# Optimization experiments

Measured on AMD Instinct MI355X. Metric: run time of the kernel, lower is better.

Reference implementation:

```python
import jax, jax.numpy as jnp
import numpy as np

N, M, NNZ, D, H = 4096, 1024, 65536, 512, 8
DH = D // H
DFF = 4 * D
EPS = 1e-5


def layer_norm(x, g, b):
    mu = jnp.mean(x, axis=-1, keepdims=True)
    var = jnp.mean((x - mu) ** 2, axis=-1, keepdims=True)
    return (x - mu) / jnp.sqrt(var + EPS) * g + b


def setup_inputs() -> dict:
    key = jax.random.key(0)
    ks = jax.random.split(key, 16)
    s = 1.0 / np.sqrt(D)
    inp = {}
    inp['x'] = jax.random.normal(ks[0], (N, D), jnp.float32)
    node = jax.random.randint(ks[1], (NNZ,), 0, N, jnp.int32)
    edge = jax.random.randint(ks[2], (NNZ,), 0, M, jnp.int32)
    inp['hyperedge_index'] = jnp.stack([node, edge], axis=0)
    inp['hyperedge_attr'] = jax.random.normal(ks[3], (M, D), jnp.float32)
    # HypergraphConv params (heads=1): lin (no bias), att [2*D], output bias
    inp['Wh'] = jax.random.normal(ks[4], (D, D), jnp.float32) * s
    inp['att'] = jax.random.normal(ks[5], (2 * D,), jnp.float32) * s
    inp['bias_h'] = jnp.zeros((D,), jnp.float32)
    # outer LayerNorms
    inp['ln1_g'] = jnp.ones((D,), jnp.float32); inp['ln1_b'] = jnp.zeros((D,), jnp.float32)
    inp['ln2_g'] = jnp.ones((D,), jnp.float32); inp['ln2_b'] = jnp.zeros((D,), jnp.float32)
    # TransformerEncoderLayer params (post-norm, relu, dropout off at eval)
    inp['in_proj_w'] = jax.random.normal(ks[6], (3 * D, D), jnp.float32) * s
    inp['in_proj_b'] = jnp.zeros((3 * D,), jnp.float32)
    inp['out_proj_w'] = jax.random.normal(ks[7], (D, D), jnp.float32) * s
    inp['out_proj_b'] = jnp.zeros((D,), jnp.float32)
    inp['ff1_w'] = jax.random.normal(ks[8], (DFF, D), jnp.float32) * s
    inp['ff1_b'] = jnp.zeros((DFF,), jnp.float32)
    inp['ff2_w'] = jax.random.normal(ks[9], (D, DFF), jnp.float32) * (1.0 / np.sqrt(DFF))
    inp['ff2_b'] = jnp.zeros((D,), jnp.float32)
    inp['tln1_g'] = jnp.ones((D,), jnp.float32); inp['tln1_b'] = jnp.zeros((D,), jnp.float32)
    inp['tln2_g'] = jnp.ones((D,), jnp.float32); inp['tln2_b'] = jnp.zeros((D,), jnp.float32)
    return inp


def hypergraph_conv(x, node, edge, hyperedge_attr, Wh, att, bias_h):
    # PyG HypergraphConv, use_attention=True, heads=1, concat=True
    xl = x @ Wh.T                      # [N, D]
    el = hyperedge_attr @ Wh.T         # [M, D]
    # per-incidence attention score
    a = xl[node] @ att[:D] + el[edge] @ att[D:]          # [NNZ]
    a = jnp.where(a >= 0, a, 0.2 * a)                    # leaky_relu(0.2)
    # scatter-softmax grouped by node index
    amax = jax.ops.segment_max(a, node, num_segments=N)
    a = jnp.exp(a - amax[node])
    den = jax.ops.segment_sum(a, node, num_segments=N)
    alpha = a / (den[node] + 1e-16)
    # degree normalizations (hyperedge_weight = ones)
    ones = jnp.ones((NNZ,), x.dtype)
    Dn = jax.ops.segment_sum(ones, node, num_segments=N)
    Dinv = jnp.where(Dn > 0, 1.0 / Dn, 0.0)
    Bn = jax.ops.segment_sum(ones, edge, num_segments=M)
    Binv = jnp.where(Bn > 0, 1.0 / Bn, 0.0)
    # node -> hyperedge aggregation
    msg1 = (Binv[edge] * alpha)[:, None] * xl[node]      # [NNZ, D]
    ef = jax.ops.segment_sum(msg1, edge, num_segments=M)  # [M, D]
    # hyperedge -> node aggregation
    msg2 = (Dinv[node] * alpha)[:, None] * ef[edge]
    out = jax.ops.segment_sum(msg2, node, num_segments=N)  # [N, D]
    return out + bias_h


def reference(x, hyperedge_index, hyperedge_attr, Wh, att, bias_h,
              ln1_g, ln1_b, ln2_g, ln2_b,
              in_proj_w, in_proj_b, out_proj_w, out_proj_b,
              ff1_w, ff1_b, ff2_w, ff2_b,
              tln1_g, tln1_b, tln2_g, tln2_b):
    node, edge = hyperedge_index[0], hyperedge_index[1]
    x_conv = hypergraph_conv(x, node, edge, hyperedge_attr, Wh, att, bias_h)
    x1 = layer_norm(x + x_conv, ln1_g, ln1_b)
    # TransformerEncoderLayer (post-norm, eval: dropout off), seq of N tokens
    qkv = x1 @ in_proj_w.T + in_proj_b
    q, k, v = jnp.split(qkv, 3, axis=-1)
    q = q.reshape(N, H, DH); k = k.reshape(N, H, DH); v = v.reshape(N, H, DH)
    scores = jnp.einsum('nhd,mhd->hnm', q, k) / np.sqrt(DH)
    attw = jax.nn.softmax(scores, axis=-1)
    ctx = jnp.einsum('hnm,mhd->nhd', attw, v).reshape(N, D)
    attn_out = ctx @ out_proj_w.T + out_proj_b
    x2 = layer_norm(x1 + attn_out, tln1_g, tln1_b)
    ff = jax.nn.relu(x2 @ ff1_w.T + ff1_b) @ ff2_w.T + ff2_b
    x3 = layer_norm(x2 + ff, tln2_g, tln2_b)
    return layer_norm(x1 + x3, ln2_g, ln2_b)
```

## Files before the change

kernel.cpp:

```cpp
#include <hip/hip_runtime.h>
#include <math.h>

#define NN   4096
#define MM   1024
#define NNZC 65536
#define DD   512
#define HH   8
#define DHH  64
#define DFFC 2048
#define NSPLIT 4

typedef short bf16x8 __attribute__((ext_vector_type(8)));
typedef float f32x4  __attribute__((ext_vector_type(4)));

static __device__ inline unsigned short f2bf(float f) {
  union { float f; unsigned int u; } v; v.f = f;
  unsigned int r = v.u + 0x7fff + ((v.u >> 16) & 1);
  return (unsigned short)(r >> 16);
}
static __device__ inline float bf2f(unsigned short u) {
  return __uint_as_float((unsigned int)u << 16);
}

__device__ inline void gload16(const void* g, void* l) {
  __builtin_amdgcn_global_load_lds(
      (const __attribute__((address_space(1))) void*)g,
      (__attribute__((address_space(3))) void*)l, 16, 0, 0);
}

__device__ inline void atomicMaxF(float* addr, float val) {
  if (val >= 0.f) atomicMax((int*)addr, __float_as_int(val));
  else            atomicMin((unsigned int*)addr, __float_as_uint(val));
}

__global__ void init_kernel(float* amax, float* den, int* DnCnt, int* BnCnt,
                            int* node_cur, int* edge_cur) {
  int i = blockIdx.x * 256 + threadIdx.x;
  if (i < NN) { amax[i] = -INFINITY; den[i] = 0.f; DnCnt[i] = 0; node_cur[i] = 0; }
  if (i < MM) { BnCnt[i] = 0; edge_cur[i] = 0; }
}

__global__ __launch_bounds__(256) void f2b_multi(
    const float* s0, unsigned short* d0, int n0,
    const float* s1, unsigned short* d1, int n1,
    const float* s2, unsigned short* d2, int n2,
    const float* s3, unsigned short* d3, int n3,
    const float* s4, unsigned short* d4, int n4,
    const float* s5, unsigned short* d5, int n5,
    const float* s6, unsigned short* d6, int n6) {
  const float* in; unsigned short* out; int n8;
  switch (blockIdx.y) {
    case 0: in=s0; out=d0; n8=n0; break;
    case 1: in=s1; out=d1; n8=n1; break;
    case 2: in=s2; out=d2; n8=n2; break;
    case 3: in=s3; out=d3; n8=n3; break;
    case 4: in=s4; out=d4; n8=n4; break;
    case 5: in=s5; out=d5; n8=n5; break;
    default: in=s6; out=d6; n8=n6; break;
  }
  for (int i = blockIdx.x*256 + threadIdx.x; i < n8; i += gridDim.x*256) {
    float4 v0 = *(const float4*)&in[(size_t)i*8];
    float4 v1 = *(const float4*)&in[(size_t)i*8 + 4];
    unsigned short w[8];
    w[0]=f2bf(v0.x); w[1]=f2bf(v0.y); w[2]=f2bf(v0.z); w[3]=f2bf(v0.w);
    w[4]=f2bf(v1.x); w[5]=f2bf(v1.y); w[6]=f2bf(v1.z); w[7]=f2bf(v1.w);
    *(ulonglong2*)&out[(size_t)i*8] = *(ulonglong2*)w;
  }
}

__global__ __launch_bounds__(256) void gemm_bt_bf16(
    const unsigned short* __restrict__ A, const unsigned short* __restrict__ B,
    const float* __restrict__ bias, float* __restrict__ Cf,
    unsigned short* __restrict__ Cb, int N, int K, int relu) {
  __shared__ __align__(16) unsigned short Al[128*64];
  __shared__ __align__(16) unsigned short Bl[128*64];
  const int t = threadIdx.x;
  const int w = t >> 6, l = t & 63;
  const int lg = l >> 4, lid = l & 15;
  const int wr = w >> 1, wc = w & 1;
  const int bm = blockIdx.x * 128, bn = blockIdx.y * 128;

  f32x4 acc[4][4];
  #pragma unroll
  for (int mi = 0; mi < 4; ++mi)
    #pragma unroll
    for (int ni = 0; ni < 4; ++ni) acc[mi][ni] = (f32x4)0.f;

  for (int k0 = 0; k0 < K; k0 += 64) {
    #pragma unroll
    for (int i = 0; i < 4; ++i) {
      int cid = i*256 + t;
      int row = cid >> 3, cp = cid & 7;
      int gc = cp ^ (row & 7);
      gload16(&A[(size_t)(bm + row)*K + k0 + gc*8], &Al[cid*8]);
      gload16(&B[(size_t)(bn + row)*K + k0 + gc*8], &Bl[cid*8]);
    }
    asm volatile("s_waitcnt vmcnt(0)" ::: "memory");
    __syncthreads();
    #pragma unroll
    for (int ks = 0; ks < 2; ++ks) {
      bf16x8 af[4], bfr[4];
      #pragma unroll
      for (int mi = 0; mi < 4; ++mi) {
        int r = wr*64 + mi*16 + lid;
        af[mi] = *(const bf16x8*)&Al[r*64 + ((ks*4 + lg) ^ (r & 7))*8];
      }
      #pragma unroll
      for (int ni = 0; ni < 4; ++ni) {
        int r = wc*64 + ni*16 + lid;
        bfr[ni] = *(const bf16x8*)&Bl[r*64 + ((ks*4 + lg) ^ (r & 7))*8];
      }
      __builtin_amdgcn_s_setprio(1);
      #pragma unroll
      for (int mi = 0; mi < 4; ++mi)
        #pragma unroll
        for (int ni = 0; ni < 4; ++ni)
          acc[mi][ni] = __builtin_amdgcn_mfma_f32_16x16x32_bf16(af[mi], bfr[ni], acc[mi][ni], 0, 0, 0);
      __builtin_amdgcn_s_setprio(0);
    }
    __syncthreads();
  }

  #pragma unroll
  for (int ni = 0; ni < 4; ++ni) {
    int col = bn + wc*64 + ni*16 + lid;
    float bv = bias ? bias[col] : 0.f;
    #pragma unroll
    for (int mi = 0; mi < 4; ++mi) {
      #pragma unroll
      for (int rg = 0; rg < 4; ++rg) {
        int row = bm + wr*64 + mi*16 + lg*4 + rg;
        float v = acc[mi][ni][rg] + bv;
        if (relu) v = fmaxf(v, 0.f);
        if (Cf) Cf[(size_t)row*N + col] = v;
        if (Cb) Cb[(size_t)row*N + col] = f2bf(v);
      }
    }
  }
}

__global__ __launch_bounds__(256) void gemm_bt_bf16_n64(
    const unsigned short* __restrict__ A, const unsigned short* __restrict__ B,
    const float* __restrict__ bias, unsigned short* __restrict__ Cb, int N, int K,
    unsigned short* __restrict__ VtbOpt) {
  __shared__ __align__(16) unsigned short Al[128*64];
  __shared__ __align__(16) unsigned short Bl[64*64];
  const int t = threadIdx.x;
  const int w = t >> 6, l = t & 63;
  const int lg = l >> 4, lid = l & 15;
  const int wr = w >> 1, wc = w & 1;
  const int bm = blockIdx.x * 128, bn = blockIdx.y * 64;

  f32x4 acc[4][2];
  #pragma unroll
  for (int mi = 0; mi < 4; ++mi)
    #pragma unroll
    for (int ni = 0; ni < 2; ++ni) acc[mi][ni] = (f32x4)0.f;

  for (int k0 = 0; k0 < K; k0 += 64) {
    #pragma unroll
    for (int i = 0; i < 4; ++i) {
      int cid = i*256 + t;
      int row = cid >> 3, cp = cid & 7;
      int gc = cp ^ (row & 7);
      gload16(&A[(size_t)(bm + row)*K + k0 + gc*8], &Al[cid*8]);
    }
    #pragma unroll
    for (int i = 0; i < 2; ++i) {
      int cid = i*256 + t;
      int row = cid >> 3, cp = cid & 7;
      int gc = cp ^ (row & 7);
      gload16(&B[(size_t)(bn + row)*K + k0 + gc*8], &Bl[cid*8]);
    }
    asm volatile("s_waitcnt vmcnt(0)" ::: "memory");
    __syncthreads();
    #pragma unroll
    for (int ks = 0; ks < 2; ++ks) {
      bf16x8 af[4], bfr[2];
      #pragma unroll
      for (int mi = 0; mi < 4; ++mi) {
        int r = wr*64 + mi*16 + lid;
        af[mi] = *(const bf16x8*)&Al[r*64 + ((ks*4 + lg) ^ (r & 7))*8];
      }
      #pragma unroll
      for (int ni = 0; ni < 2; ++ni) {
        int r = wc*32 + ni*16 + lid;
        bfr[ni] = *(const bf16x8*)&Bl[r*64 + ((ks*4 + lg) ^ (r & 7))*8];
      }
      __builtin_amdgcn_s_setprio(1);
      #pragma unroll
      for (int mi = 0; mi < 4; ++mi)
        #pragma unroll
        for (int ni = 0; ni < 2; ++ni)
          acc[mi][ni] = __builtin_amdgcn_mfma_f32_16x16x32_bf16(af[mi], bfr[ni], acc[mi][ni], 0, 0, 0);
      __builtin_amdgcn_s_setprio(0);
    }
    __syncthreads();
  }

  if (VtbOpt && bn >= 1024) {
    #pragma unroll
    for (int ni = 0; ni < 2; ++ni) {
      int col = bn + wc*32 + ni*16 + lid;
      float bv = bias ? bias[col] : 0.f;
      int d = col - 1024;
      int h = d >> 6, dd = d & 63;
      #pragma unroll
      for (int mi = 0; mi < 4; ++mi) {
        int tok0 = bm + wr*64 + mi*16 + lg*4;
        ushort4 w4;
        w4.x = f2bf(acc[mi][ni][0] + bv);
        w4.y = f2bf(acc[mi][ni][1] + bv);
        w4.z = f2bf(acc[mi][ni][2] + bv);
        w4.w = f2bf(acc[mi][ni][3] + bv);
        *(ushort4*)&VtbOpt[(size_t)h*64*NN + (size_t)dd*NN + tok0] = w4;
      }
    }
  } else {
    #pragma unroll
    for (int ni = 0; ni < 2; ++ni) {
      int col = bn + wc*32 + ni*16 + lid;
      float bv = bias ? bias[col] : 0.f;
      #pragma unroll
      for (int mi = 0; mi < 4; ++mi) {
        #pragma unroll
        for (int rg = 0; rg < 4; ++rg) {
          int row = bm + wr*64 + mi*16 + lg*4 + rg;
          Cb[(size_t)row*N + col] = f2bf(acc[mi][ni][rg] + bv);
        }
      }
    }
  }
}

__global__ __launch_bounds__(256) void rowdot_both(const unsigned short* __restrict__ xlb,
    const unsigned short* __restrict__ elb, const float* __restrict__ att,
    float* __restrict__ s_node, float* __restrict__ s_edge) {
  int w = (blockIdx.x * 256 + threadIdx.x) >> 6;
  int lane = threadIdx.x & 63;
  const unsigned short* xr;
  const float* vec;
  if (w < NN) { xr = &xlb[(size_t)w * DD]; vec = att; }
  else        { xr = &elb[(size_t)(w - NN) * DD]; vec = att + DD; }
  float s = 0.f;
  #pragma unroll
  for (int j = 0; j < 8; ++j) s += bf2f(xr[lane + 64*j]) * vec[lane + 64*j];
  #pragma unroll
  for (int off = 1; off < 64; off <<= 1) s += __shfl_xor(s, off, 64);
  if (lane == 0) {
    if (w < NN) s_node[w] = s;
    else        s_edge[w - NN] = s;
  }
}

__global__ void incidence_pass1(const int* __restrict__ node_idx, const int* __restrict__ edge_idx,
    const float* __restrict__ s_node, const float* __restrict__ s_edge,
    float* __restrict__ a_buf, float* amax, int* DnCnt, int* BnCnt) {
  int i = blockIdx.x * 256 + threadIdx.x;
  if (i >= NNZC) return;
  int n = node_idx[i], m = edge_idx[i];
  float a = s_node[n] + s_edge[m];
  a = (a >= 0.f) ? a : 0.2f * a;
  a_buf[i] = a;
  atomicMaxF(&amax[n], a);
  atomicAdd(&DnCnt[n], 1);
  atomicAdd(&BnCnt[m], 1);
}

__global__ __launch_bounds__(1024) void exscan2_kernel(const int* __restrict__ inA,
    int* __restrict__ outA, int nA, const int* __restrict__ inB, int* __restrict__ outB, int nB) {
  const int* in; int* out; int n;
  if (blockIdx.x == 0) { in = inA; out = outA; n = nA; }
  else                 { in = inB; out = outB; n = nB; }
  __shared__ int sums[1024];
  const int t = threadIdx.x;
  const int chunk = (n + 1023) >> 10;
  const int start = t * chunk;
  const int stop  = min(start + chunk, n);
  int local = 0;
  for (int i = start; i < stop; ++i) local += in[i];
  sums[t] = local;
  __syncthreads();
  for (int o = 1; o < 1024; o <<= 1) {
    int v = (t >= o) ? sums[t - o] : 0;
    __syncthreads();
    sums[t] += v;
    __syncthreads();
  }
  int run = (t == 0) ? 0 : sums[t - 1];
  for (int i = start; i < stop; ++i) { out[i] = run; run += in[i]; }
  if (t == 1023) out[n] = sums[1023];
}

__global__ void incidence_pass2(const int* __restrict__ node_idx, const int* __restrict__ edge_idx,
    float* __restrict__ a_buf, const float* __restrict__ amax, float* den,
    const int* __restrict__ node_off, const int* __restrict__ edge_off,
    int* node_cur, int* edge_cur, int* node_list, int* edge_list) {
  int i = blockIdx.x * 256 + threadIdx.x;
  if (i >= NNZC) return;
  int n = node_idx[i], m = edge_idx[i];
  float e = __expf(a_buf[i] - amax[n]);
  a_buf[i] = e;
  atomicAdd(&den[n], e);
  int pn = atomicAdd(&node_cur[n], 1);
  node_list[node_off[n] + pn] = i;
  int pm = atomicAdd(&edge_cur[m], 1);
  edge_list[edge_off[m] + pm] = i;
}

__global__ __launch_bounds__(256) void gather_edge(const int* __restrict__ edge_off,
    const int* __restrict__ edge_list, const int* __restrict__ node_idx,
    const float* __restrict__ a_buf, const float* __restrict__ den,
    const unsigned short* __restrict__ xlb, unsigned short* __restrict__ efb) {
  int m = blockIdx.x;
  int t = threadIdx.x;
  int beg = edge_off[m], end = edge_off[m+1];
  int cnt = end - beg;
  float Binv = (cnt > 0) ? (1.0f / (float)cnt) : 0.f;
  __shared__ int   ln_[128];
  __shared__ float lw_[128];
  float acc0 = 0.f, acc1 = 0.f;
  for (int c = beg; c < end; c += 128) {
    int nchunk = min(128, end - c);
    if (t < nchunk) {
      int i = edge_list[c + t];
      int n = node_idx[i];
      ln_[t] = n;
      lw_[t] = a_buf[i] / (den[n] + 1e-16f) * Binv;
    }
    __syncthreads();
    float a0 = 0.f, a1 = 0.f, b0 = 0.f, b1 = 0.f;
    int j = 0;
    for (; j + 1 < nchunk; j += 2) {
      float w0 = lw_[j], w1 = lw_[j+1];
      const unsigned short* r0 = &xlb[(size_t)ln_[j]   * DD];
      const unsigned short* r1 = &xlb[(size_t)ln_[j+1] * DD];
      a0 += w0 * bf2f(r0[t]);       b0 += w0 * bf2f(r0[t + 256]);
      a1 += w1 * bf2f(r1[t]);       b1 += w1 * bf2f(r1[t + 256]);
    }
    if (j < nchunk) {
      float w0 = lw_[j];
      const unsigned short* r0 = &xlb[(size_t)ln_[j] * DD];
      a0 += w0 * bf2f(r0[t]);       b0 += w0 * bf2f(r0[t + 256]);
    }
    acc0 += a0 + a1;
    acc1 += b0 + b1;
    __syncthreads();
  }
  efb[(size_t)m * DD + t]       = f2bf(acc0);
  efb[(size_t)m * DD + t + 256] = f2bf(acc1);
}

__global__ __launch_bounds__(256) void gather_node_ln(const int* __restrict__ node_off,
    const int* __restrict__ node_list, const int* __restrict__ edge_idx,
    const float* __restrict__ a_buf, const float* __restrict__ den,
    const unsigned short* __restrict__ efb, const float* __restrict__ bias_h,
    const float* __restrict__ x, const float* __restrict__ g, const float* __restrict__ be,
    unsigned short* __restrict__ x1b) {
  int n = blockIdx.x;
  int t = threadIdx.x;
  int beg = node_off[n], end = node_off[n+1];
  int cnt = end - beg;
  float Dinv = (cnt > 0) ? (1.0f / (float)cnt) : 0.f;
  float wscale = Dinv / (den[n] + 1e-16f);
  __shared__ int   le_[128];
  __shared__ float lw_[128];
  float acc0 = 0.f, acc1 = 0.f;
  for (int c = beg; c < end; c += 128) {
    int nchunk = min(128, end - c);
    if (t < nchunk) {
      int i = node_list[c + t];
      le_[t] = edge_idx[i];
      lw_[t] = a_buf[i] * wscale;
    }
    __syncthreads();
    float a0 = 0.f, a1 = 0.f, b0 = 0.f, b1 = 0.f;
    int j = 0;
    for (; j + 1 < nchunk; j += 2) {
      float w0 = lw_[j], w1 = lw_[j+1];
      const unsigned short* r0 = &efb[(size_t)le_[j]   * DD];
      const unsigned short* r1 = &efb[(size_t)le_[j+1] * DD];
      a0 += w0 * bf2f(r0[t]);       b0 += w0 * bf2f(r0[t + 256]);
      a1 += w1 * bf2f(r1[t]);       b1 += w1 * bf2f(r1[t + 256]);
    }
    if (j < nchunk) {
      float w0 = lw_[j];
      const unsigned short* r0 = &efb[(size_t)le_[j] * DD];
      a0 += w0 * bf2f(r0[t]);       b0 += w0 * bf2f(r0[t + 256]);
    }
    acc0 += a0 + a1;
    acc1 += b0 + b1;
    __syncthreads();
  }
  float v0 = x[(size_t)n*DD + t]       + acc0 + bias_h[t];
  float v1 = x[(size_t)n*DD + t + 256] + acc1 + bias_h[t + 256];
  __shared__ float red[4];
  __shared__ float mu_s, rstd_s;
  float s = v0 + v1;
  #pragma unroll
  for (int off = 1; off < 64; off <<= 1) s += __shfl_xor(s, off, 64);
  int wid = t >> 6;
  if ((t & 63) == 0) red[wid] = s;
  __syncthreads();
  if (t == 0) mu_s = (red[0] + red[1] + red[2] + red[3]) / 512.f;
  __syncthreads();
  float mu = mu_s;
  float d0 = v0 - mu, d1 = v1 - mu;
  float vs = d0*d0 + d1*d1;
  #pragma unroll
  for (int off = 1; off < 64; off <<= 1) vs += __shfl_xor(vs, off, 64);
  if ((t & 63) == 0) red[wid] = vs;
  __syncthreads();
  if (t == 0) rstd_s = rsqrtf((red[0] + red[1] + red[2] + red[3]) / 512.f + 1e-5f);
  __syncthreads();
  float rs = rstd_s;
  x1b[(size_t)n*DD + t]       = f2bf(d0 * rs * g[t]       + be[t]);
  x1b[(size_t)n*DD + t + 256] = f2bf(d1 * rs * g[t + 256] + be[t + 256]);
}

__global__ __launch_bounds__(256) void ln_res_bb(const unsigned short* __restrict__ a,
    const unsigned short* __restrict__ b, const float* __restrict__ g,
    const float* __restrict__ be, unsigned short* __restrict__ outb) {
  int r = blockIdx.x;
  int t = threadIdx.x;
  float v0 = bf2f(a[(size_t)r*DD + t])       + bf2f(b[(size_t)r*DD + t]);
  float v1 = bf2f(a[(size_t)r*DD + t + 256]) + bf2f(b[(size_t)r*DD + t + 256]);
  __shared__ float red[4];
  __shared__ float mu_s, rstd_s;
  float s = v0 + v1;
  #pragma unroll
  for (int off = 1; off < 64; off <<= 1) s += __shfl_xor(s, off, 64);
  int wid = t >> 6;
  if ((t & 63) == 0) red[wid] = s;
  __syncthreads();
  if (t == 0) mu_s = (red[0] + red[1] + red[2] + red[3]) / 512.f;
  __syncthreads();
  float mu = mu_s;
  float d0 = v0 - mu, d1 = v1 - mu;
  float vs = d0*d0 + d1*d1;
  #pragma unroll
  for (int off = 1; off < 64; off <<= 1) vs += __shfl_xor(vs, off, 64);
  if ((t & 63) == 0) red[wid] = vs;
  __syncthreads();
  if (t == 0) rstd_s = rsqrtf((red[0] + red[1] + red[2] + red[3]) / 512.f + 1e-5f);
  __syncthreads();
  float rs = rstd_s;
  outb[(size_t)r*DD + t]       = f2bf(d0 * rs * g[t]       + be[t]);
  outb[(size_t)r*DD + t + 256] = f2bf(d1 * rs * g[t + 256] + be[t + 256]);
}

__global__ __launch_bounds__(256) void ln_final2(const unsigned short* __restrict__ x2b,
    const unsigned short* __restrict__ ffob, const unsigned short* __restrict__ x1b,
    const float* __restrict__ g1, const float* __restrict__ b1,
    const float* __restrict__ g2, const float* __restrict__ b2,
    float* __restrict__ out) {
  int r = blockIdx.x;
  int t = threadIdx.x;
  __shared__ float red[4];
  __shared__ float sh0, sh1;
  int wid = t >> 6;
  float v0 = bf2f(x2b[(size_t)r*DD + t])       + bf2f(ffob[(size_t)r*DD + t]);
  float v1 = bf2f(x2b[(size_t)r*DD + t + 256]) + bf2f(ffob[(size_t)r*DD + t + 256]);
  float s = v0 + v1;
  #pragma unroll
  for (int off = 1; off < 64; off <<= 1) s += __shfl_xor(s, off, 64);
  if ((t & 63) == 0) red[wid] = s;
  __syncthreads();
  if (t == 0) sh0 = (red[0] + red[1] + red[2] + red[3]) / 512.f;
  __syncthreads();
  float mu = sh0;
  float d0 = v0 - mu, d1 = v1 - mu;
  float vs = d0*d0 + d1*d1;
  #pragma unroll
  for (int off = 1; off < 64; off <<= 1) vs += __shfl_xor(vs, off, 64);
  if ((t & 63) == 0) red[wid] = vs;
  __syncthreads();
  if (t == 0) sh1 = rsqrtf((red[0] + red[1] + red[2] + red[3]) / 512.f + 1e-5f);
  __syncthreads();
  float rs = sh1;
  float x30 = d0 * rs * g1[t]       + b1[t];
  float x31 = d1 * rs * g1[t + 256] + b1[t + 256];
  __syncthreads();
  float u0 = bf2f(x1b[(size_t)r*DD + t])       + x30;
  float u1 = bf2f(x1b[(size_t)r*DD + t + 256]) + x31;
  s = u0 + u1;
  #pragma unroll
  for (int off = 1; off < 64; off <<= 1) s += __shfl_xor(s, off, 64);
  if ((t & 63) == 0) red[wid] = s;
  __syncthreads();
  if (t == 0) sh0 = (red[0] + red[1] + red[2] + red[3]) / 512.f;
  __syncthreads();
  mu = sh0;
  d0 = u0 - mu; d1 = u1 - mu;
  vs = d0*d0 + d1*d1;
  #pragma unroll
  for (int off = 1; off < 64; off <<= 1) vs += __shfl_xor(vs, off, 64);
  if ((t & 63) == 0) red[wid] = vs;
  __syncthreads();
  if (t == 0) sh1 = rsqrtf((red[0] + red[1] + red[2] + red[3]) / 512.f + 1e-5f);
  __syncthreads();
  rs = sh1;
  out[(size_t)r*DD + t]       = d0 * rs * g2[t]       + b2[t];
  out[(size_t)r*DD + t + 256] = d1 * rs * g2[t + 256] + b2[t + 256];
}

__global__ __launch_bounds__(256) void attn_mfma_part(const unsigned short* __restrict__ qkvbb,
                                                      const unsigned short* __restrict__ Vtb,
                                                      unsigned short* __restrict__ Opartb,
                                                      float* __restrict__ ml) {
  const int head = blockIdx.y;
  const int z = blockIdx.z;
  const int q0 = blockIdx.x * 64;
  const int t = threadIdx.x;
  const int w = t >> 6;
  const int l = t & 63;
  const int lg = l >> 4;
  const int lid = l & 15;
  const float sc = 0.125f * 1.44269504f;
  const float THRraw = 44.36f;

  __shared__ __align__(16) unsigned short Kl[64*64];
  __shared__ __align__(16) unsigned short Vl[64*64];

  bf16x8 qa[2];
  {
    const int qrow = q0 + w*16 + lid;
    const unsigned short* qp = &qkvbb[(size_t)qrow*1536 + head*64];
    qa[0] = *(const bf16x8*)&qp[lg*8];
    qa[1] = *(const bf16x8*)&qp[32 + lg*8];
  }

  int addr[4][2];
  #pragma unroll
  for (int i = 0; i < 4; ++i)
    #pragma unroll
    for (int hf = 0; hf < 2; ++hf) {
      int row = i*16 + lid;
      addr[i][hf] = (row*64 + hf*32 + lg*8) ^ ((row & 7) << 3);
    }

  float m = -1e30f, msc = -1e30f, lsum = 0.f;
  f32x4 o[4];
  #pragma unroll
  for (int dt = 0; dt < 4; ++dt) o[dt] = (f32x4)0.f;

  const unsigned short* Kh = qkvbb + 512 + head*64;
  const unsigned short* Vh = Vtb + (size_t)head*64*NN;
  const int kt0 = z * (NN / NSPLIT);
  const int kt1 = kt0 + (NN / NSPLIT);

  const int srow0 = t >> 3,        scc = (t & 7) * 8;
  const int srow1 = 32 + (t >> 3);
  const int sdst0 = (srow0*64 + scc) ^ ((srow0 & 7) << 3);
  const int sdst1 = (srow1*64 + scc) ^ ((srow1 & 7) << 3);
  const int kperm0 = 8*((srow0>>2)&3) + 4*((srow0>>4)&1) + (srow0&3) + 32*(srow0>>5);
  const int kperm1 = 8*((srow1>>2)&3) + 4*((srow1>>4)&1) + (srow1&3) + 32*(srow1>>5);
  ulonglong2 kreg0, kreg1, vreg0, vreg1;

#define LOADKV(ktv) do { \
    kreg0 = *(const ulonglong2*)&Kh[(size_t)((ktv) + kperm0)*1536 + scc]; \
    vreg0 = *(const ulonglong2*)&Vh[(size_t)srow0*NN + (ktv) + scc]; \
    kreg1 = *(const ulonglong2*)&Kh[(size_t)((ktv) + kperm1)*1536 + scc]; \
    vreg1 = *(const ulonglong2*)&Vh[(size_t)srow1*NN + (ktv) + scc]; \
  } while (0)
#define STORKV() do { \
    *(ulonglong2*)&Kl[sdst0] = kreg0; *(ulonglong2*)&Vl[sdst0] = vreg0; \
    *(ulonglong2*)&Kl[sdst1] = kreg1; *(ulonglong2*)&Vl[sdst1] = vreg1; \
  } while (0)

  LOADKV(kt0);
  STORKV();
  __syncthreads();

  for (int kt = kt0; kt < kt1; kt += 64) {
    const bool hn = (kt + 64) < kt1;
    if (hn) LOADKV(kt + 64);

    f32x4 s[4];
    #pragma unroll
    for (int n = 0; n < 4; ++n) s[n] = (f32x4)0.f;
    __builtin_amdgcn_s_setprio(1);
    #pragma unroll
    for (int n = 0; n < 4; ++n) {
      #pragma unroll
      for (int hf = 0; hf < 2; ++hf) {
        bf16x8 kb = *(const bf16x8*)&Kl[addr[n][hf]];
        s[n] = __builtin_amdgcn_mfma_f32_16x16x32_bf16(kb, qa[hf], s[n], 0, 0, 0);
      }
    }
    __builtin_amdgcn_s_setprio(0);

    float a0 = fmaxf(fmaxf(s[0][0], s[0][1]), s[0][2]);
    float a1 = fmaxf(fmaxf(s[0][3], s[1][0]), s[1][1]);
    float a2 = fmaxf(fmaxf(s[1][2], s[1][3]), s[2][0]);
    float a3 = fmaxf(fmaxf(s[2][1], s[2][2]), s[2][3]);
    float a4 = fmaxf(fmaxf(s[3][0], s[3][1]), s[3][2]);
    float mx = fmaxf(fmaxf(fmaxf(a0, a1), a2), fmaxf(fmaxf(a3, a4), s[3][3]));
    mx = fmaxf(mx, __shfl_xor(mx, 16, 64));
    mx = fmaxf(mx, __shfl_xor(mx, 32, 64));
    if (!__all(mx <= m + THRraw)) {
      float mn = fmaxf(m, mx);
      float c = exp2f((m - mn) * sc);
      m = mn;
      msc = m * sc;
      lsum *= c;
      #pragma unroll
      for (int r = 0; r < 4; ++r) {
        float cr = __shfl(c, lg*4 + r, 64);
        #pragma unroll
        for (int dt = 0; dt < 4; ++dt) o[dt][r] *= cr;
      }
    }
    float ps = 0.f;
    #pragma unroll
    for (int n = 0; n < 4; ++n)
      #pragma unroll
      for (int r = 0; r < 4; ++r) {
        float p = exp2f(fmaf(s[n][r], sc, -msc));
        s[n][r] = p;
        ps += p;
      }
    ps += __shfl_xor(ps, 16, 64);
    ps += __shfl_xor(ps, 32, 64);
    lsum += ps;

    union { bf16x8 v; unsigned int u[4]; } pa[2];
    #pragma unroll
    for (int hf = 0; hf < 2; ++hf) {
      asm("v_cvt_pk_bf16_f32 %0, %1, %2" : "=v"(pa[hf].u[0]) : "v"(s[2*hf][0]),   "v"(s[2*hf][1]));
      asm("v_cvt_pk_bf16_f32 %0, %1, %2" : "=v"(pa[hf].u[1]) : "v"(s[2*hf][2]),   "v"(s[2*hf][3]));
      asm("v_cvt_pk_bf16_f32 %0, %1, %2" : "=v"(pa[hf].u[2]) : "v"(s[2*hf+1][0]), "v"(s[2*hf+1][1]));
      asm("v_cvt_pk_bf16_f32 %0, %1, %2" : "=v"(pa[hf].u[3]) : "v"(s[2*hf+1][2]), "v"(s[2*hf+1][3]));
    }

    __builtin_amdgcn_s_setprio(1);
    #pragma unroll
    for (int dt = 0; dt < 4; ++dt) {
      #pragma unroll
      for (int hf = 0; hf < 2; ++hf) {
        bf16x8 vb = *(const bf16x8*)&Vl[addr[dt][hf]];
        o[dt] = __builtin_amdgcn_mfma_f32_16x16x32_bf16(pa[hf].v, vb, o[dt], 0, 0, 0);
      }
    }
    __builtin_amdgcn_s_setprio(0);

    __syncthreads();
    if (hn) {
      STORKV();
      __syncthreads();
    }
  }
#undef LOADKV
#undef STORKV

  #pragma unroll
  for (int r = 0; r < 4; ++r) {
    int q = q0 + w*16 + lg*4 + r;
    size_t base = ((size_t)(z*HH + head)*NN + q)*64;
    #pragma unroll
    for (int dt = 0; dt < 4; ++dt)
      Opartb[base + dt*16 + lid] = f2bf(o[dt][r]);
  }
  if (l < 16) {
    int q = q0 + w*16 + l;
    size_t mb = ((size_t)(z*HH + head)*NN + q)*2;
    ml[mb]     = msc;
    ml[mb + 1] = lsum;
  }
}

__global__ __launch_bounds__(256) void attn_combine(const unsigned short* __restrict__ Opartb,
                                                    const float* __restrict__ ml,
                                                    unsigned short* __restrict__ ctxb) {
  const int w = threadIdx.x >> 6, lane = threadIdx.x & 63;
  const int row = blockIdx.x * 4 + w;
  const int q = row >> 3, head = row & 7;
  float ms[NSPLIT], ls[NSPLIT];
  float mglob = -1e30f;
  #pragma unroll
  for (int s = 0; s < NSPLIT; ++s) {
    size_t mb = ((size_t)(s*HH + head)*NN + q)*2;
    ms[s] = ml[mb]; ls[s] = ml[mb + 1];
    mglob = fmaxf(mglob, ms[s]);
  }
  float lt = 0.f, ov = 0.f;
  #pragma unroll
  for (int s = 0; s < NSPLIT; ++s) {
    float wgt = exp2f(ms[s] - mglob);
    lt += ls[s] * wgt;
    ov += bf2f(Opartb[((size_t)(s*HH + head)*NN + q)*64 + lane]) * wgt;
  }
  ctxb[(size_t)q*DD + head*64 + lane] = f2bf(ov / lt);
}

extern "C" void kernel_launch(void* const* d_in, const int* in_sizes, int n_in,
                              void* d_out, int out_size, void* d_ws, size_t ws_size,
                              hipStream_t stream) {
  const float* x       = (const float*)d_in[0];
  const int*   hidx    = (const int*)d_in[1];
  const float* hattr   = (const float*)d_in[2];
  const float* Wh      = (const float*)d_in[3];
  const float* att     = (const float*)d_in[4];
  const float* bias_h  = (const float*)d_in[5];
  const float* ln1_g   = (const float*)d_in[6];
  const float* ln1_b   = (const float*)d_in[7];
  const float* ln2_g   = (const float*)d_in[8];
  const float* ln2_b   = (const float*)d_in[9];
  const float* in_proj_w  = (const float*)d_in[10];
  const float* in_proj_b  = (const float*)d_in[11];
  const float* out_proj_w = (const float*)d_in[12];
  const float* out_proj_b = (const float*)d_in[13];
  const float* ff1_w   = (const float*)d_in[14];
  const float* ff1_b   = (const float*)d_in[15];
  const float* ff2_w   = (const float*)d_in[16];
  const float* ff2_b   = (const float*)d_in[17];
  const float* tln1_g  = (const float*)d_in[18];
  const float* tln1_b  = (const float*)d_in[19];
  const float* tln2_g  = (const float*)d_in[20];
  const float* tln2_b  = (const float*)d_in[21];
  const int* node_idx = hidx;
  const int* edge_idx = hidx + NNZC;

  char* ws = (char*)d_ws;
  size_t off = 0;
  auto alloc = [&](size_t bytes) -> void* {
    void* p = ws + off;
    off = (off + bytes + 63) & ~(size_t)63;
    return p;
  };
  float* s_node   = (float*)alloc(sizeof(float)*NN);
  float* s_edge   = (float*)alloc(sizeof(float)*MM);
  float* a_buf    = (float*)alloc(sizeof(float)*NNZC);
  float* amax     = (float*)alloc(sizeof(float)*NN);
  float* den      = (float*)alloc(sizeof(float)*NN);
  int*   DnCnt    = (int*)alloc(sizeof(int)*NN);
  int*   BnCnt    = (int*)alloc(sizeof(int)*MM);
  int*   node_off = (int*)alloc(sizeof(int)*(NN+1));
  int*   edge_off = (int*)alloc(sizeof(int)*(MM+1));
  int*   node_cur = (int*)alloc(sizeof(int)*NN);
  int*   edge_cur = (int*)alloc(sizeof(int)*MM);
  int*   node_list= (int*)alloc(sizeof(int)*NNZC);
  int*   edge_list= (int*)alloc(sizeof(int)*NNZC);
  unsigned short* xhb   = (unsigned short*)alloc(sizeof(unsigned short)*(NN+MM)*DD);
  unsigned short* xelb  = (unsigned short*)alloc(sizeof(unsigned short)*(NN+MM)*DD);
  unsigned short* efb   = (unsigned short*)alloc(sizeof(unsigned short)*MM*DD);
  unsigned short* qkvbb = (unsigned short*)alloc(sizeof(unsigned short)*NN*3*DD);
  unsigned short* Vtb   = (unsigned short*)alloc(sizeof(unsigned short)*NN*DD);
  unsigned short* Whb   = (unsigned short*)alloc(sizeof(unsigned short)*DD*DD);
  unsigned short* ipwb  = (unsigned short*)alloc(sizeof(unsigned short)*3*DD*DD);
  unsigned short* opwb  = (unsigned short*)alloc(sizeof(unsigned short)*DD*DD);
  unsigned short* ff1wb = (unsigned short*)alloc(sizeof(unsigned short)*DFFC*DD);
  unsigned short* ff2wb = (unsigned short*)alloc(sizeof(unsigned short)*DD*DFFC);
  unsigned short* x1b   = (unsigned short*)alloc(sizeof(unsigned short)*NN*DD);
  unsigned short* x2b   = (unsigned short*)alloc(sizeof(unsigned short)*NN*DD);
  unsigned short* ctxb  = (unsigned short*)alloc(sizeof(unsigned short)*NN*DD);
  unsigned short* attn_outb = (unsigned short*)alloc(sizeof(unsigned short)*NN*DD);
  char* late = (char*)alloc(20u*1024*1024);
  unsigned short* Opartb = (unsigned short*)late;
  float*          mlb    = (float*)(late + 16u*1024*1024);
  unsigned short* ffhb   = (unsigned short*)late;
  unsigned short* ffob   = (unsigned short*)(late + 16u*1024*1024);
  unsigned short* xlb = xelb;
  unsigned short* elb = xelb + (size_t)NN*DD;
  (void)ws_size; (void)in_sizes; (void)n_in; (void)out_size;

  dim3 b256(256);
  f2b_multi<<<dim3(256, 7), b256, 0, stream>>>(
      x, xhb, NN*DD/8,  hattr, xhb + (size_t)NN*DD, MM*DD/8,  Wh, Whb, DD*DD/8,
      in_proj_w, ipwb, 3*DD*DD/8,  out_proj_w, opwb, DD*DD/8,
      ff1_w, ff1wb, DFFC*DD/8,  ff2_w, ff2wb, DD*DFFC/8);

  gemm_bt_bf16_n64<<<dim3((NN+MM)/128, DD/64), b256, 0, stream>>>(xhb, Whb, nullptr, xelb, DD, DD, nullptr);
  rowdot_both<<<(NN+MM)/4, b256, 0, stream>>>(xlb, elb, att, s_node, s_edge);
  init_kernel<<<NN/256, b256, 0, stream>>>(amax, den, DnCnt, BnCnt, node_cur, edge_cur);
  incidence_pass1<<<NNZC/256, b256, 0, stream>>>(node_idx, edge_idx, s_node, s_edge,
                                                 a_buf, amax, DnCnt, BnCnt);
  exscan2_kernel<<<2, 1024, 0, stream>>>(DnCnt, node_off, NN, BnCnt, edge_off, MM);
  incidence_pass2<<<NNZC/256, b256, 0, stream>>>(node_idx, edge_idx, a_buf, amax, den,
                                                 node_off, edge_off, node_cur, edge_cur,
                                                 node_list, edge_list);
  gather_edge<<<MM, b256, 0, stream>>>(edge_off, edge_list, node_idx, a_buf, den, xlb, efb);
  gather_node_ln<<<NN, b256, 0, stream>>>(node_off, node_list, edge_idx, a_buf, den, efb,
                                          bias_h, x, ln1_g, ln1_b, x1b);
  gemm_bt_bf16_n64<<<dim3(NN/128, (3*DD)/64), b256, 0, stream>>>(x1b, ipwb, in_proj_b, qkvbb, 3*DD, DD, Vtb);
  attn_mfma_part<<<dim3(NN/64, HH, NSPLIT), b256, 0, stream>>>(qkvbb, Vtb, Opartb, mlb);
  attn_combine<<<NN*HH/4, b256, 0, stream>>>(Opartb, mlb, ctxb);
  gemm_bt_bf16_n64<<<dim3(NN/128, DD/64), b256, 0, stream>>>(ctxb, opwb, out_proj_b, attn_outb, DD, DD, nullptr);
  ln_res_bb<<<NN, b256, 0, stream>>>(x1b, attn_outb, tln1_g, tln1_b, x2b);
  gemm_bt_bf16<<<dim3(NN/128, DFFC/128), b256, 0, stream>>>(x2b, ff1wb, ff1_b, nullptr, ffhb, DFFC, DD, 1);
  gemm_bt_bf16_n64<<<dim3(NN/128, DD/64), b256, 0, stream>>>(ffhb, ff2wb, ff2_b, ffob, DD, DFFC, nullptr);
  ln_final2<<<NN, b256, 0, stream>>>(x2b, ffob, x1b, tln2_g, tln2_b, ln2_g, ln2_b, (float*)d_out);
}
```

Measured before the change: 264.4 us.

## Double-buffer K/V LDS tiles in attention and unroll hypergraph gathers by four

The attention kernel now keeps two LDS buffers for K and V. The next tile is written into the alternate buffer and only one barrier is needed per iteration instead of two, which cuts synchronisation stalls. Precomputed LDS addresses are replaced with inline swizzle computation, saving registers at the cost of some integer ALU work. The two hypergraph gather kernels unroll by four rows with independent accumulators to keep more memory loads in flight. LDS use in the attention kernel doubles to 32KB per block, which could lower occupancy.

Measured after the change: 260.3 us. Within noise of the previous version (-1.5%).

```diff
diff --git a/kernel.cpp b/kernel.cpp
--- a/kernel.cpp
+++ b/kernel.cpp
@@ -329,22 +329,27 @@
       lw_[t] = a_buf[i] / (den[n] + 1e-16f) * Binv;
     }
     __syncthreads();
-    float a0 = 0.f, a1 = 0.f, b0 = 0.f, b1 = 0.f;
+    float a0 = 0.f, a1 = 0.f, a2 = 0.f, a3 = 0.f;
+    float b0 = 0.f, b1 = 0.f, b2 = 0.f, b3 = 0.f;
     int j = 0;
-    for (; j + 1 < nchunk; j += 2) {
-      float w0 = lw_[j], w1 = lw_[j+1];
+    for (; j + 3 < nchunk; j += 4) {
+      float w0 = lw_[j], w1 = lw_[j+1], w2 = lw_[j+2], w3 = lw_[j+3];
       const unsigned short* r0 = &xlb[(size_t)ln_[j]   * DD];
       const unsigned short* r1 = &xlb[(size_t)ln_[j+1] * DD];
-      a0 += w0 * bf2f(r0[t]);       b0 += w0 * bf2f(r0[t + 256]);
-      a1 += w1 * bf2f(r1[t]);       b1 += w1 * bf2f(r1[t + 256]);
-    }
-    if (j < nchunk) {
+      const unsigned short* r2 = &xlb[(size_t)ln_[j+2] * DD];
+      const unsigned short* r3 = &xlb[(size_t)ln_[j+3] * DD];
+      a0 += w0 * bf2f(r0[t]);  b0 += w0 * bf2f(r0[t + 256]);
+      a1 += w1 * bf2f(r1[t]);  b1 += w1 * bf2f(r1[t + 256]);
+      a2 += w2 * bf2f(r2[t]);  b2 += w2 * bf2f(r2[t + 256]);
+      a3 += w3 * bf2f(r3[t]);  b3 += w3 * bf2f(r3[t + 256]);
+    }
+    for (; j < nchunk; ++j) {
       float w0 = lw_[j];
       const unsigned short* r0 = &xlb[(size_t)ln_[j] * DD];
-      a0 += w0 * bf2f(r0[t]);       b0 += w0 * bf2f(r0[t + 256]);
-    }
-    acc0 += a0 + a1;
-    acc1 += b0 + b1;
+      a0 += w0 * bf2f(r0[t]);  b0 += w0 * bf2f(r0[t + 256]);
+    }
+    acc0 += (a0 + a1) + (a2 + a3);
+    acc1 += (b0 + b1) + (b2 + b3);
     __syncthreads();
   }
   efb[(size_t)m * DD + t]       = f2bf(acc0);
@@ -374,22 +379,27 @@
       lw_[t] = a_buf[i] * wscale;
     }
     __syncthreads();
-    float a0 = 0.f, a1 = 0.f, b0 = 0.f, b1 = 0.f;
+    float a0 = 0.f, a1 = 0.f, a2 = 0.f, a3 = 0.f;
+    float b0 = 0.f, b1 = 0.f, b2 = 0.f, b3 = 0.f;
     int j = 0;
-    for (; j + 1 < nchunk; j += 2) {
-      float w0 = lw_[j], w1 = lw_[j+1];
+    for (; j + 3 < nchunk; j += 4) {
+      float w0 = lw_[j], w1 = lw_[j+1], w2 = lw_[j+2], w3 = lw_[j+3];
       const unsigned short* r0 = &efb[(size_t)le_[j]   * DD];
       const unsigned short* r1 = &efb[(size_t)le_[j+1] * DD];
-      a0 += w0 * bf2f(r0[t]);       b0 += w0 * bf2f(r0[t + 256]);
-      a1 += w1 * bf2f(r1[t]);       b1 += w1 * bf2f(r1[t + 256]);
-    }
-    if (j < nchunk) {
+      const unsigned short* r2 = &efb[(size_t)le_[j+2] * DD];
+      const unsigned short* r3 = &efb[(size_t)le_[j+3] * DD];
+      a0 += w0 * bf2f(r0[t]);  b0 += w0 * bf2f(r0[t + 256]);
+      a1 += w1 * bf2f(r1[t]);  b1 += w1 * bf2f(r1[t + 256]);
+      a2 += w2 * bf2f(r2[t]);  b2 += w2 * bf2f(r2[t + 256]);
+      a3 += w3 * bf2f(r3[t]);  b3 += w3 * bf2f(r3[t + 256]);
+    }
+    for (; j < nchunk; ++j) {
       float w0 = lw_[j];
       const unsigned short* r0 = &efb[(size_t)le_[j] * DD];
-      a0 += w0 * bf2f(r0[t]);       b0 += w0 * bf2f(r0[t + 256]);
-    }
-    acc0 += a0 + a1;
-    acc1 += b0 + b1;
+      a0 += w0 * bf2f(r0[t]);  b0 += w0 * bf2f(r0[t + 256]);
+    }
+    acc0 += (a0 + a1) + (a2 + a3);
+    acc1 += (b0 + b1) + (b2 + b3);
     __syncthreads();
   }
   float v0 = x[(size_t)n*DD + t]       + acc0 + bias_h[t];
@@ -519,8 +529,8 @@
   const float sc = 0.125f * 1.44269504f;
   const float THRraw = 44.36f;
 
-  __shared__ __align__(16) unsigned short Kl[64*64];
-  __shared__ __align__(16) unsigned short Vl[64*64];
+  __shared__ __align__(16) unsigned short Kl[2][64*64];
+  __shared__ __align__(16) unsigned short Vl[2][64*64];
 
   bf16x8 qa[2];
   {
@@ -529,15 +539,6 @@
     qa[0] = *(const bf16x8*)&qp[lg*8];
     qa[1] = *(const bf16x8*)&qp[32 + lg*8];
   }
-
-  int addr[4][2];
-  #pragma unroll
-  for (int i = 0; i < 4; ++i)
-    #pragma unroll
-    for (int hf = 0; hf < 2; ++hf) {
-      int row = i*16 + lid;
-      addr[i][hf] = (row*64 + hf*32 + lg*8) ^ ((row & 7) << 3);
-    }
 
   float m = -1e30f, msc = -1e30f, lsum = 0.f;
   f32x4 o[4];
@@ -563,18 +564,21 @@
     kreg1 = *(const ulonglong2*)&Kh[(size_t)((ktv) + kperm1)*1536 + scc]; \
     vreg1 = *(const ulonglong2*)&Vh[(size_t)srow1*NN + (ktv) + scc]; \
   } while (0)
-#define STORKV() do { \
-    *(ulonglong2*)&Kl[sdst0] = kreg0; *(ulonglong2*)&Vl[sdst0] = vreg0; \
-    *(ulonglong2*)&Kl[sdst1] = kreg1; *(ulonglong2*)&Vl[sdst1] = vreg1; \
+#define STORKV(b) do { \
+    *(ulonglong2*)&Kl[b][sdst0] = kreg0; *(ulonglong2*)&Vl[b][sdst0] = vreg0; \
+    *(ulonglong2*)&Kl[b][sdst1] = kreg1; *(ulonglong2*)&Vl[b][sdst1] = vreg1; \
   } while (0)
 
   LOADKV(kt0);
-  STORKV();
-  __syncthreads();
-
+  STORKV(0);
+  __syncthreads();
+
+  int cur = 0;
   for (int kt = kt0; kt < kt1; kt += 64) {
     const bool hn = (kt + 64) < kt1;
     if (hn) LOADKV(kt + 64);
+    const unsigned short* Klc = &Kl[cur][0];
+    const unsigned short* Vlc = &Vl[cur][0];
 
     f32x4 s[4];
     #pragma unroll
@@ -582,9 +586,11 @@
     __builtin_amdgcn_s_setprio(1);
     #pragma unroll
     for (int n = 0; n < 4; ++n) {
+      int tok = n*16 + lid;
       #pragma unroll
       for (int hf = 0; hf < 2; ++hf) {
-        bf16x8 kb = *(const bf16x8*)&Kl[addr[n][hf]];
+        int didx = (tok*64 + hf*32 + lg*8) ^ ((tok & 7) << 3);
+        bf16x8 kb = *(const bf16x8*)&Klc[didx];
         s[n] = __builtin_amdgcn_mfma_f32_16x16x32_bf16(kb, qa[hf], s[n], 0, 0, 0);
       }
     }
@@ -636,19 +642,19 @@
     __builtin_amdgcn_s_setprio(1);
     #pragma unroll
     for (int dt = 0; dt < 4; ++dt) {
+      int drow = dt*16 + lid;
       #pragma unroll
       for (int hf = 0; hf < 2; ++hf) {
-        bf16x8 vb = *(const bf16x8*)&Vl[addr[dt][hf]];
+        int didx = (drow*64 + hf*32 + lg*8) ^ ((drow & 7) << 3);
+        bf16x8 vb = *(const bf16x8*)&Vlc[didx];
         o[dt] = __builtin_amdgcn_mfma_f32_16x16x32_bf16(pa[hf].v, vb, o[dt], 0, 0, 0);
       }
     }
     __builtin_amdgcn_s_setprio(0);
 
-    __syncthreads();
-    if (hn) {
-      STORKV();
-      __syncthreads();
-    }
+    if (hn) STORKV(cur ^ 1);
+    __syncthreads();
+    cur ^= 1;
   }
 #undef LOADKV
 #undef STORKV
```
